# Kernel tuning notes

Hardware: AMD Instinct MI355X
Metric: run time of the kernel (lower is better)

Reference implementation:

```python
import jax, jax.numpy as jnp
import numpy as np

B, M, E = 8192, 200, 64
OTHER = 128
FEA = 256  # E + E + OTHER
ADIM = 3 * E


def setup_inputs() -> dict:
    key = jax.random.key(0)
    ks = jax.random.split(key, 12)
    s = lambda fan: 1.0 / np.sqrt(fan)
    return {
        "hist": jax.random.normal(ks[0], (B, M, E), jnp.float32),
        "target": jax.random.normal(ks[1], (B, E), jnp.float32),
        "other": jax.random.normal(ks[2], (B, OTHER), jnp.float32),
        "aW1": jax.random.normal(ks[3], (ADIM, ADIM // 2), jnp.float32) * s(ADIM),
        "ab1": jnp.zeros((ADIM // 2,), jnp.float32),
        "aW2": jax.random.normal(ks[4], (ADIM // 2, 1), jnp.float32) * s(ADIM // 2),
        "ab2": jnp.zeros((1,), jnp.float32),
        "oW1": jax.random.normal(ks[5], (FEA, FEA // 2), jnp.float32) * s(FEA),
        "ob1": jnp.zeros((FEA // 2,), jnp.float32),
        "oW2": jax.random.normal(ks[6], (FEA // 2, FEA // 3), jnp.float32) * s(FEA // 2),
        "ob2": jnp.zeros((FEA // 3,), jnp.float32),
        "oW3": jax.random.normal(ks[7], (FEA // 3, FEA // 4), jnp.float32) * s(FEA // 3),
        "ob3": jnp.zeros((FEA // 4,), jnp.float32),
        "fW": jax.random.normal(ks[8], (FEA // 4, 1), jnp.float32) * s(FEA // 4),
        "fb": jnp.zeros((1,), jnp.float32),
    }


def reference(hist, target, other, aW1, ab1, aW2, ab2,
              oW1, ob1, oW2, ob2, oW3, ob3, fW, fb):
    # DIN activation unit, vectorized over the m history steps.
    tgt = target[:, None, :]                                  # [B,1,E]
    a = jnp.concatenate(
        [hist, hist * tgt, jnp.broadcast_to(tgt, hist.shape)], axis=-1
    )                                                          # [B,M,3E]
    h = jax.nn.relu(jnp.einsum("bma,ah->bmh", a, aW1) + ab1)   # [B,M,3E/2]
    aij = jnp.einsum("bmh,ho->bmo", h, aW2) + ab2              # [B,M,1]
    tmp = jnp.sum(aij * hist, axis=1)                          # [B,E]

    x = jnp.concatenate([tmp, target, other], axis=1)          # [B,FEA]
    x = jax.nn.relu(x @ oW1 + ob1)
    x = jax.nn.relu(x @ oW2 + ob2)
    x = jax.nn.relu(x @ oW3 + ob3)
    out = jax.nn.sigmoid(x @ fW + fb)                          # [B,1]
    return out
```

## Files before the change

kernel.cpp:

```cpp
#include <hip/hip_runtime.h>
#include <math.h>

#define BATCH 8192
#define M 200
#define E 64
#define H1 96
#define F1 128
#define F2 85
#define F3 64
#define SH 72
#define MT 13

typedef _Float16 half8_t __attribute__((ext_vector_type(8)));
typedef float floatx4 __attribute__((ext_vector_type(4)));

__global__ __launch_bounds__(256, 4) void din_kernel(
    const float* __restrict__ hist, const float* __restrict__ target,
    const float* __restrict__ other,
    const float* __restrict__ aW1, const float* __restrict__ ab1,
    const float* __restrict__ aW2, const float* __restrict__ ab2,
    const float* __restrict__ oW1, const float* __restrict__ ob1,
    const float* __restrict__ oW2, const float* __restrict__ ob2,
    const float* __restrict__ oW3, const float* __restrict__ ob3,
    const float* __restrict__ fW,  const float* __restrict__ fb,
    float* __restrict__ out)
{
    __shared__ _Float16 WbT[H1 * SH];
    __shared__ float tgtS[E];
    __shared__ float beS[H1];
    __shared__ float aW2S[H1];
    __shared__ float xS[256];
    __shared__ float scr[512];
    __shared__ float h1S[F1];
    __shared__ float h2S[F2];
    __shared__ float ab2S;

    const int t = threadIdx.x;
    const int b = blockIdx.x;
    const int lane = t & 63;
    const int wv   = t >> 6;
    const int quad = lane >> 4;
    const int lm   = lane & 15;

    {
    }
    int mt = wv;
    const int row0  = mt * 16 + lm;
    const int rowc0 = row0 < M ? row0 : (M - 1);
    const float4* p0 = (const float4*)(hist + ((size_t)b * M + rowc0) * E + quad * 8);
    float4 f0 = p0[0], g0 = p0[1], f1 = p0[8], g1 = p0[9];
    float oth = 0.f;
    if (t >= 128) oth = other[(size_t)b * 128 + (t - 128)];

    if (t < E) tgtS[t] = target[(size_t)b * E + t];
    if (t == 0) ab2S = ab2[0];
    __syncthreads();

    for (int idx = t; idx < E * H1; idx += 256) {
        int k = idx / H1, j = idx - k * H1;
        float w = aW1[idx] + tgtS[k] * aW1[E * H1 + idx];
        WbT[j * SH + k] = (_Float16)w;
    }
    if (t < H1) {
        float s0 = ab1[t], s1 = 0.f, s2 = 0.f, s3 = 0.f;
        const float* wp = aW1 + (size_t)(2 * E) * H1 + t;
        #pragma unroll 4
        for (int k = 0; k < E; k += 4) {
            s0 += tgtS[k]     * wp[(size_t)k * H1];
            s1 += tgtS[k + 1] * wp[(size_t)(k + 1) * H1];
            s2 += tgtS[k + 2] * wp[(size_t)(k + 2) * H1];
            s3 += tgtS[k + 3] * wp[(size_t)(k + 3) * H1];
        }
        beS[t] = (s0 + s1) + (s2 + s3);
        aW2S[t] = aW2[t];
    }
    __syncthreads();

    half8_t bf[12];
    #pragma unroll
    for (int nt = 0; nt < 6; ++nt) {
        #pragma unroll
        for (int kk = 0; kk < 2; ++kk)
            bf[nt * 2 + kk] =
                *(const half8_t*)&WbT[(nt * 16 + lm) * SH + kk * 32 + quad * 8];
    }
    float beR[6], w2R[6];
    #pragma unroll
    for (int nt = 0; nt < 6; ++nt) {
        beR[nt] = beS[nt * 16 + lm];
        w2R[nt] = aW2S[nt * 16 + lm];
    }

    float tk0[8], tk1[8];
    #pragma unroll
    for (int j = 0; j < 8; ++j) { tk0[j] = 0.f; tk1[j] = 0.f; }

    const int qs16 = (lm >> 2) << 4;
    const int rsel = lm & 3;

    for (; mt < MT; mt += 4) {
        const int nmt = mt + 4;
        float4 nf0 = f0, ng0 = g0, nf1 = f1, ng1 = g1;
        if (nmt < MT) {
            const int nrow  = nmt * 16 + lm;
            const int nrowc = nrow < M ? nrow : (M - 1);
            const float4* np = (const float4*)(hist + ((size_t)b * M + nrowc) * E + quad * 8);
            nf0 = np[0]; ng0 = np[1]; nf1 = np[8]; ng1 = np[9];
        }

        const int m0  = mt * 16;
        const int row = m0 + lm;
        half8_t a0 = { (_Float16)f0.x, (_Float16)f0.y, (_Float16)f0.z, (_Float16)f0.w,
                       (_Float16)g0.x, (_Float16)g0.y, (_Float16)g0.z, (_Float16)g0.w };
        half8_t a1 = { (_Float16)f1.x, (_Float16)f1.y, (_Float16)f1.z, (_Float16)f1.w,
                       (_Float16)g1.x, (_Float16)g1.y, (_Float16)g1.z, (_Float16)g1.w };

        float s0 = 0.f, s1 = 0.f, s2 = 0.f, s3 = 0.f;
        #pragma unroll
        for (int nt = 0; nt < 6; ++nt) {
            floatx4 acc = {0.f, 0.f, 0.f, 0.f};
            acc = __builtin_amdgcn_mfma_f32_16x16x32_f16(a0, bf[nt * 2],     acc, 0, 0, 0);
            acc = __builtin_amdgcn_mfma_f32_16x16x32_f16(a1, bf[nt * 2 + 1], acc, 0, 0, 0);
            float be_n = beR[nt];
            float w2   = w2R[nt];
            s0 += fmaxf(acc[0] + be_n, 0.f) * w2;
            s1 += fmaxf(acc[1] + be_n, 0.f) * w2;
            s2 += fmaxf(acc[2] + be_n, 0.f) * w2;
            s3 += fmaxf(acc[3] + be_n, 0.f) * w2;
        }
        #pragma unroll
        for (int off = 1; off < 16; off <<= 1) {
            s0 += __shfl_xor(s0, off);
            s1 += __shfl_xor(s1, off);
            s2 += __shfl_xor(s2, off);
            s3 += __shfl_xor(s3, off);
        }
        float v0 = __shfl(s0, qs16), v1 = __shfl(s1, qs16);
        float v2 = __shfl(s2, qs16), v3 = __shfl(s3, qs16);
        float aij = (rsel == 0) ? v0 : (rsel == 1) ? v1 : (rsel == 2) ? v2 : v3;
        aij += ab2S;
        aij = (row < M) ? aij : 0.f;

        tk0[0] += f0.x * aij; tk0[1] += f0.y * aij;
        tk0[2] += f0.z * aij; tk0[3] += f0.w * aij;
        tk0[4] += g0.x * aij; tk0[5] += g0.y * aij;
        tk0[6] += g0.z * aij; tk0[7] += g0.w * aij;
        tk1[0] += f1.x * aij; tk1[1] += f1.y * aij;
        tk1[2] += f1.z * aij; tk1[3] += f1.w * aij;
        tk1[4] += g1.x * aij; tk1[5] += g1.y * aij;
        tk1[6] += g1.z * aij; tk1[7] += g1.w * aij;

        f0 = nf0; g0 = ng0; f1 = nf1; g1 = ng1;
    }

    #pragma unroll
    for (int j = 0; j < 8; ++j) {
        #pragma unroll
        for (int off = 1; off < 16; off <<= 1) {
            tk0[j] += __shfl_xor(tk0[j], off);
            tk1[j] += __shfl_xor(tk1[j], off);
        }
    }
    if (lm == 0) {
        #pragma unroll
        for (int j = 0; j < 8; ++j) {
            scr[wv * E + quad * 8 + j]      = tk0[j];
            scr[wv * E + 32 + quad * 8 + j] = tk1[j];
        }
    }
    __syncthreads();

    if (t < 64)
        xS[t] = (scr[t] + scr[64 + t]) + (scr[128 + t] + scr[192 + t]);
    else if (t < 128)
        xS[t] = tgtS[t - 64];
    else
        xS[t] = oth;
    __syncthreads();

    {
        const int g = t & 31, s = t >> 5;
        const float* wbase = oW1 + 4 * g;
        const int c0 = s * 32;
        float ax = 0.f, ay = 0.f, az = 0.f, aw = 0.f;
        #pragma unroll 8
        for (int i = 0; i < 32; ++i) {
            const int c = c0 + i;
            float xv = xS[c];
            float4 w4 = *(const float4*)(wbase + (size_t)c * F1);
            ax += xv * w4.x; ay += xv * w4.y;
            az += xv * w4.z; aw += xv * w4.w;
        }
        ax += __shfl_xor(ax, 32);
        ay += __shfl_xor(ay, 32);
        az += __shfl_xor(az, 32);
        aw += __shfl_xor(aw, 32);
        if (lane < 32) {
            float4 r = { ax, ay, az, aw };
            *(float4*)&scr[wv * 128 + 4 * g] = r;
        }
    }
    __syncthreads();
    if (t < F1)
        h1S[t] = fmaxf((scr[t] + scr[128 + t]) + (scr[256 + t] + scr[384 + t]) + ob1[t], 0.f);
    __syncthreads();

    {
        const int o = t & 127, ph = t >> 7;
        if (o < F2) {
            float sA = 0.f, sB = 0.f;
            const int c0 = ph * 64;
            #pragma unroll 8
            for (int c = 0; c < 64; c += 2) {
                sA += h1S[c0 + c]     * oW2[(size_t)(c0 + c) * F2 + o];
                sB += h1S[c0 + c + 1] * oW2[(size_t)(c0 + c + 1) * F2 + o];
            }
            scr[ph * 128 + o] = sA + sB;
        }
    }
    __syncthreads();
    if (t < F2) h2S[t] = fmaxf(scr[t] + scr[128 + t] + ob2[t], 0.f);
    __syncthreads();

    {
        const int o = t & 63, ph = t >> 6;
        const int c0 = (85 * ph) >> 2, c1 = (85 * (ph + 1)) >> 2;
        float s = 0.f;
        for (int c = c0; c < c1; ++c)
            s += h2S[c] * oW3[(size_t)c * F3 + o];
        scr[ph * 64 + o] = s;
    }
    __syncthreads();

    if (t < 64) {
        float v = fmaxf((scr[t] + scr[64 + t]) + (scr[128 + t] + scr[192 + t]) + ob3[t], 0.f) * fW[t];
        v += __shfl_xor(v, 1);  v += __shfl_xor(v, 2);  v += __shfl_xor(v, 4);
        v += __shfl_xor(v, 8);  v += __shfl_xor(v, 16); v += __shfl_xor(v, 32);
        if (t == 0) out[b] = 1.f / (1.f + __expf(-(v + fb[0])));
    }
}

extern "C" void kernel_launch(void* const* d_in, const int* in_sizes, int n_in,
                              void* d_out, int out_size, void* d_ws, size_t ws_size,
                              hipStream_t stream) {
    const float* hist   = (const float*)d_in[0];
    const float* target = (const float*)d_in[1];
    const float* other  = (const float*)d_in[2];
    const float* aW1    = (const float*)d_in[3];
    const float* ab1    = (const float*)d_in[4];
    const float* aW2    = (const float*)d_in[5];
    const float* ab2    = (const float*)d_in[6];
    const float* oW1    = (const float*)d_in[7];
    const float* ob1    = (const float*)d_in[8];
    const float* oW2    = (const float*)d_in[9];
    const float* ob2    = (const float*)d_in[10];
    const float* oW3    = (const float*)d_in[11];
    const float* ob3    = (const float*)d_in[12];
    const float* fW     = (const float*)d_in[13];
    const float* fb     = (const float*)d_in[14];
    float* out = (float*)d_out;

    din_kernel<<<BATCH, 256, 0, stream>>>(hist, target, other,
                                          aW1, ab1, aW2, ab2,
                                          oW1, ob1, oW2, ob2, oW3, ob3,
                                          fW, fb, out);
}
```

Baseline: 743.9 us.

## Process two history tiles per iteration and read MFMA B fragments from LDS

Each wave now loads and processes two 16-row history tiles per loop step, at rows mt and mt+64, and prefetches the next pair. This doubles the global loads in flight to hide memory latency. To pay for the extra registers, the MFMA B fragments, bias and aW2 values are read from shared memory inside the loop instead of being held in registers. The launch bounds are replaced with an explicit waves_per_eu(4,4) attribute. The cost is extra LDS reads per tile and some wasted clamped loads for rows past M.

```diff
diff --git a/kernel.cpp b/kernel.cpp
--- a/kernel.cpp
+++ b/kernel.cpp
@@ -14,7 +14,9 @@
 typedef _Float16 half8_t __attribute__((ext_vector_type(8)));
 typedef float floatx4 __attribute__((ext_vector_type(4)));
 
-__global__ __launch_bounds__(256, 4) void din_kernel(
+__global__ __launch_bounds__(256)
+__attribute__((amdgpu_waves_per_eu(4, 4)))
+void din_kernel(
     const float* __restrict__ hist, const float* __restrict__ target,
     const float* __restrict__ other,
     const float* __restrict__ aW1, const float* __restrict__ ab1,
@@ -42,13 +44,13 @@
     const int quad = lane >> 4;
     const int lm   = lane & 15;
 
-    {
-    }
-    int mt = wv;
-    const int row0  = mt * 16 + lm;
-    const int rowc0 = row0 < M ? row0 : (M - 1);
-    const float4* p0 = (const float4*)(hist + ((size_t)b * M + rowc0) * E + quad * 8);
-    float4 f0 = p0[0], g0 = p0[1], f1 = p0[8], g1 = p0[9];
+    const float* histB = hist + (size_t)b * M * E + quad * 8;
+    int rowA = wv * 16 + lm;
+    int rowB = rowA + 64;
+    const float4* pA = (const float4*)(histB + (size_t)(rowA < M ? rowA : M - 1) * E);
+    const float4* pB = (const float4*)(histB + (size_t)(rowB < M ? rowB : M - 1) * E);
+    float4 fA0 = pA[0], gA0 = pA[1], fA1 = pA[8], gA1 = pA[9];
+    float4 fB0 = pB[0], gB0 = pB[1], fB1 = pB[8], gB1 = pB[9];
     float oth = 0.f;
     if (t >= 128) oth = other[(size_t)b * 128 + (t - 128)];
 
@@ -76,53 +78,30 @@
     }
     __syncthreads();
 
-    half8_t bf[12];
-    #pragma unroll
-    for (int nt = 0; nt < 6; ++nt) {
-        #pragma unroll
-        for (int kk = 0; kk < 2; ++kk)
-            bf[nt * 2 + kk] =
-                *(const half8_t*)&WbT[(nt * 16 + lm) * SH + kk * 32 + quad * 8];
-    }
-    float beR[6], w2R[6];
-    #pragma unroll
-    for (int nt = 0; nt < 6; ++nt) {
-        beR[nt] = beS[nt * 16 + lm];
-        w2R[nt] = aW2S[nt * 16 + lm];
-    }
+    const _Float16* bfB = &WbT[lm * SH + quad * 8];
+    const int qs16 = (lm >> 2) << 4;
+    const int rsel = lm & 3;
 
     float tk0[8], tk1[8];
     #pragma unroll
     for (int j = 0; j < 8; ++j) { tk0[j] = 0.f; tk1[j] = 0.f; }
 
-    const int qs16 = (lm >> 2) << 4;
-    const int rsel = lm & 3;
-
-    for (; mt < MT; mt += 4) {
-        const int nmt = mt + 4;
-        float4 nf0 = f0, ng0 = g0, nf1 = f1, ng1 = g1;
-        if (nmt < MT) {
-            const int nrow  = nmt * 16 + lm;
-            const int nrowc = nrow < M ? nrow : (M - 1);
-            const float4* np = (const float4*)(hist + ((size_t)b * M + nrowc) * E + quad * 8);
-            nf0 = np[0]; ng0 = np[1]; nf1 = np[8]; ng1 = np[9];
-        }
-
-        const int m0  = mt * 16;
-        const int row = m0 + lm;
+    auto tile_aij = [&](const float4& f0, const float4& g0,
+                        const float4& f1, const float4& g1, int row) -> float {
         half8_t a0 = { (_Float16)f0.x, (_Float16)f0.y, (_Float16)f0.z, (_Float16)f0.w,
                        (_Float16)g0.x, (_Float16)g0.y, (_Float16)g0.z, (_Float16)g0.w };
         half8_t a1 = { (_Float16)f1.x, (_Float16)f1.y, (_Float16)f1.z, (_Float16)f1.w,
                        (_Float16)g1.x, (_Float16)g1.y, (_Float16)g1.z, (_Float16)g1.w };
-
         float s0 = 0.f, s1 = 0.f, s2 = 0.f, s3 = 0.f;
         #pragma unroll
         for (int nt = 0; nt < 6; ++nt) {
+            half8_t b0 = *(const half8_t*)(bfB + nt * (16 * SH));
+            half8_t b1 = *(const half8_t*)(bfB + nt * (16 * SH) + 32);
             floatx4 acc = {0.f, 0.f, 0.f, 0.f};
-            acc = __builtin_amdgcn_mfma_f32_16x16x32_f16(a0, bf[nt * 2],     acc, 0, 0, 0);
-            acc = __builtin_amdgcn_mfma_f32_16x16x32_f16(a1, bf[nt * 2 + 1], acc, 0, 0, 0);
-            float be_n = beR[nt];
-            float w2   = w2R[nt];
+            acc = __builtin_amdgcn_mfma_f32_16x16x32_f16(a0, b0, acc, 0, 0, 0);
+            acc = __builtin_amdgcn_mfma_f32_16x16x32_f16(a1, b1, acc, 0, 0, 0);
+            float be_n = beS[nt * 16 + lm];
+            float w2   = aW2S[nt * 16 + lm];
             s0 += fmaxf(acc[0] + be_n, 0.f) * w2;
             s1 += fmaxf(acc[1] + be_n, 0.f) * w2;
             s2 += fmaxf(acc[2] + be_n, 0.f) * w2;
@@ -139,18 +118,46 @@
         float v2 = __shfl(s2, qs16), v3 = __shfl(s3, qs16);
         float aij = (rsel == 0) ? v0 : (rsel == 1) ? v1 : (rsel == 2) ? v2 : v3;
         aij += ab2S;
-        aij = (row < M) ? aij : 0.f;
-
-        tk0[0] += f0.x * aij; tk0[1] += f0.y * aij;
-        tk0[2] += f0.z * aij; tk0[3] += f0.w * aij;
-        tk0[4] += g0.x * aij; tk0[5] += g0.y * aij;
-        tk0[6] += g0.z * aij; tk0[7] += g0.w * aij;
-        tk1[0] += f1.x * aij; tk1[1] += f1.y * aij;
-        tk1[2] += f1.z * aij; tk1[3] += f1.w * aij;
-        tk1[4] += g1.x * aij; tk1[5] += g1.y * aij;
-        tk1[6] += g1.z * aij; tk1[7] += g1.w * aij;
-
-        f0 = nf0; g0 = ng0; f1 = nf1; g1 = ng1;
+        return (row < M) ? aij : 0.f;
+    };
+
+    for (int mt = wv; mt < MT; mt += 8) {
+        const int nmt = mt + 8;
+        float4 nfA0 = fA0, ngA0 = gA0, nfA1 = fA1, ngA1 = gA1;
+        float4 nfB0 = fB0, ngB0 = gB0, nfB1 = fB1, ngB1 = gB1;
+        if (nmt < MT) {
+            int nrA = nmt * 16 + lm;
+            int nrB = nrA + 64;
+            const float4* npA = (const float4*)(histB + (size_t)(nrA < M ? nrA : M - 1) * E);
+            const float4* npB = (const float4*)(histB + (size_t)(nrB < M ? nrB : M - 1) * E);
+            nfA0 = npA[0]; ngA0 = npA[1]; nfA1 = npA[8]; ngA1 = npA[9];
+            nfB0 = npB[0]; ngB0 = npB[1]; nfB1 = npB[8]; ngB1 = npB[9];
+        }
+
+        const float aijA = tile_aij(fA0, gA0, fA1, gA1, rowA);
+        tk0[0] += fA0.x * aijA; tk0[1] += fA0.y * aijA;
+        tk0[2] += fA0.z * aijA; tk0[3] += fA0.w * aijA;
+        tk0[4] += gA0.x * aijA; tk0[5] += gA0.y * aijA;
+        tk0[6] += gA0.z * aijA; tk0[7] += gA0.w * aijA;
+        tk1[0] += fA1.x * aijA; tk1[1] += fA1.y * aijA;
+        tk1[2] += fA1.z * aijA; tk1[3] += fA1.w * aijA;
+        tk1[4] += gA1.x * aijA; tk1[5] += gA1.y * aijA;
+        tk1[6] += gA1.z * aijA; tk1[7] += gA1.w * aijA;
+
+        const float aijB = tile_aij(fB0, gB0, fB1, gB1, rowB);
+        tk0[0] += fB0.x * aijB; tk0[1] += fB0.y * aijB;
+        tk0[2] += fB0.z * aijB; tk0[3] += fB0.w * aijB;
+        tk0[4] += gB0.x * aijB; tk0[5] += gB0.y * aijB;
+        tk0[6] += gB0.z * aijB; tk0[7] += gB0.w * aijB;
+        tk1[0] += fB1.x * aijB; tk1[1] += fB1.y * aijB;
+        tk1[2] += fB1.z * aijB; tk1[3] += fB1.w * aijB;
+        tk1[4] += gB1.x * aijB; tk1[5] += gB1.y * aijB;
+        tk1[6] += gB1.z * aijB; tk1[7] += gB1.w * aijB;
+
+        fA0 = nfA0; gA0 = ngA0; fA1 = nfA1; gA1 = ngA1;
+        fB0 = nfB0; gB0 = ngB0; fB1 = nfB1; gB1 = ngB1;
+        rowA = nmt * 16 + lm;
+        rowB = rowA + 64;
     }
 
     #pragma unroll
```

After: 1.178 ms. 58.4% more time.

## Precompute transposed fp16 attention weights once and double MFMAs instead of per-block fold

Applied to the files above, without the earlier changes.

Adds a small prep kernel that converts the hist and hist*target slices of aW1 to transposed fp16 once into workspace, so each batch block no longer builds a target-folded weight tile in shared memory. The main kernel now forms hist*target in registers and issues four MFMAs per output tile instead of two, reading weights from global/L2 each iteration rather than holding them in registers. The software prefetch of the next hist tile is removed and the occupancy hint in launch bounds is dropped. The trade is less per-block setup and LDS work against twice the matrix ops and repeated weight loads inside the loop.

```diff
diff --git a/kernel.cpp b/kernel.cpp
--- a/kernel.cpp
+++ b/kernel.cpp
@@ -8,15 +8,24 @@
 #define F1 128
 #define F2 85
 #define F3 64
-#define SH 72
 #define MT 13
 
 typedef _Float16 half8_t __attribute__((ext_vector_type(8)));
 typedef float floatx4 __attribute__((ext_vector_type(4)));
 
-__global__ __launch_bounds__(256, 4) void din_kernel(
+__global__ void din_prep(const float* __restrict__ aW1,
+                         _Float16* __restrict__ waT, _Float16* __restrict__ wbT)
+{
+    const int n = blockIdx.x;
+    const int k = threadIdx.x;
+    waT[n * 64 + k] = (_Float16)aW1[(size_t)k * H1 + n];
+    wbT[n * 64 + k] = (_Float16)aW1[(size_t)(E + k) * H1 + n];
+}
+
+__global__ __launch_bounds__(256) void din_kernel(
     const float* __restrict__ hist, const float* __restrict__ target,
     const float* __restrict__ other,
+    const _Float16* __restrict__ waT, const _Float16* __restrict__ wbT,
     const float* __restrict__ aW1, const float* __restrict__ ab1,
     const float* __restrict__ aW2, const float* __restrict__ ab2,
     const float* __restrict__ oW1, const float* __restrict__ ob1,
@@ -25,7 +34,6 @@
     const float* __restrict__ fW,  const float* __restrict__ fb,
     float* __restrict__ out)
 {
-    __shared__ _Float16 WbT[H1 * SH];
     __shared__ float tgtS[E];
     __shared__ float beS[H1];
     __shared__ float aW2S[H1];
@@ -42,25 +50,12 @@
     const int quad = lane >> 4;
     const int lm   = lane & 15;
 
-    {
-    }
-    int mt = wv;
-    const int row0  = mt * 16 + lm;
-    const int rowc0 = row0 < M ? row0 : (M - 1);
-    const float4* p0 = (const float4*)(hist + ((size_t)b * M + rowc0) * E + quad * 8);
-    float4 f0 = p0[0], g0 = p0[1], f1 = p0[8], g1 = p0[9];
     float oth = 0.f;
     if (t >= 128) oth = other[(size_t)b * 128 + (t - 128)];
-
     if (t < E) tgtS[t] = target[(size_t)b * E + t];
     if (t == 0) ab2S = ab2[0];
     __syncthreads();
 
-    for (int idx = t; idx < E * H1; idx += 256) {
-        int k = idx / H1, j = idx - k * H1;
-        float w = aW1[idx] + tgtS[k] * aW1[E * H1 + idx];
-        WbT[j * SH + k] = (_Float16)w;
-    }
     if (t < H1) {
         float s0 = ab1[t], s1 = 0.f, s2 = 0.f, s3 = 0.f;
         const float* wp = aW1 + (size_t)(2 * E) * H1 + t;
@@ -76,53 +71,52 @@
     }
     __syncthreads();
 
-    half8_t bf[12];
-    #pragma unroll
-    for (int nt = 0; nt < 6; ++nt) {
-        #pragma unroll
-        for (int kk = 0; kk < 2; ++kk)
-            bf[nt * 2 + kk] =
-                *(const half8_t*)&WbT[(nt * 16 + lm) * SH + kk * 32 + quad * 8];
-    }
-    float beR[6], w2R[6];
-    #pragma unroll
-    for (int nt = 0; nt < 6; ++nt) {
-        beR[nt] = beS[nt * 16 + lm];
-        w2R[nt] = aW2S[nt * 16 + lm];
-    }
+    const float* histB = hist + (size_t)b * M * E + quad * 8;
+    const _Float16* waB = waT + lm * 64 + quad * 8;
+    const _Float16* wbB = wbT + lm * 64 + quad * 8;
+    const float4* tgt4 = (const float4*)tgtS;
+    const int qs16 = (lm >> 2) << 4;
+    const int rsel = lm & 3;
 
     float tk0[8], tk1[8];
     #pragma unroll
     for (int j = 0; j < 8; ++j) { tk0[j] = 0.f; tk1[j] = 0.f; }
 
-    const int qs16 = (lm >> 2) << 4;
-    const int rsel = lm & 3;
-
-    for (; mt < MT; mt += 4) {
-        const int nmt = mt + 4;
-        float4 nf0 = f0, ng0 = g0, nf1 = f1, ng1 = g1;
-        if (nmt < MT) {
-            const int nrow  = nmt * 16 + lm;
-            const int nrowc = nrow < M ? nrow : (M - 1);
-            const float4* np = (const float4*)(hist + ((size_t)b * M + nrowc) * E + quad * 8);
-            nf0 = np[0]; ng0 = np[1]; nf1 = np[8]; ng1 = np[9];
-        }
-
-        const int m0  = mt * 16;
-        const int row = m0 + lm;
+    for (int mt = wv; mt < MT; mt += 4) {
+        const int row = mt * 16 + lm;
+        const float4* p = (const float4*)(histB + (size_t)(row < M ? row : M - 1) * E);
+        float4 f0 = p[0], g0 = p[1], f1 = p[8], g1 = p[9];
+
+        float4 T0 = tgt4[quad * 2],     T1 = tgt4[quad * 2 + 1];
+        float4 T2 = tgt4[8 + quad * 2], T3 = tgt4[9 + quad * 2];
+
         half8_t a0 = { (_Float16)f0.x, (_Float16)f0.y, (_Float16)f0.z, (_Float16)f0.w,
                        (_Float16)g0.x, (_Float16)g0.y, (_Float16)g0.z, (_Float16)g0.w };
         half8_t a1 = { (_Float16)f1.x, (_Float16)f1.y, (_Float16)f1.z, (_Float16)f1.w,
                        (_Float16)g1.x, (_Float16)g1.y, (_Float16)g1.z, (_Float16)g1.w };
+        half8_t a0t = { (_Float16)(f0.x * T0.x), (_Float16)(f0.y * T0.y),
+                        (_Float16)(f0.z * T0.z), (_Float16)(f0.w * T0.w),
+                        (_Float16)(g0.x * T1.x), (_Float16)(g0.y * T1.y),
+                        (_Float16)(g0.z * T1.z), (_Float16)(g0.w * T1.w) };
+        half8_t a1t = { (_Float16)(f1.x * T2.x), (_Float16)(f1.y * T2.y),
+                        (_Float16)(f1.z * T2.z), (_Float16)(f1.w * T2.w),
+                        (_Float16)(g1.x * T3.x), (_Float16)(g1.y * T3.y),
+                        (_Float16)(g1.z * T3.z), (_Float16)(g1.w * T3.w) };
 
         float s0 = 0.f, s1 = 0.f, s2 = 0.f, s3 = 0.f;
         #pragma unroll
         for (int nt = 0; nt < 6; ++nt) {
+            half8_t wa0 = *(const half8_t*)(waB + nt * 1024);
+            half8_t wa1 = *(const half8_t*)(waB + nt * 1024 + 32);
+            half8_t wb0 = *(const half8_t*)(wbB + nt * 1024);
+            half8_t wb1 = *(const half8_t*)(wbB + nt * 1024 + 32);
             floatx4 acc = {0.f, 0.f, 0.f, 0.f};
-            acc = __builtin_amdgcn_mfma_f32_16x16x32_f16(a0, bf[nt * 2],     acc, 0, 0, 0);
-            acc = __builtin_amdgcn_mfma_f32_16x16x32_f16(a1, bf[nt * 2 + 1], acc, 0, 0, 0);
-            float be_n = beR[nt];
-            float w2   = w2R[nt];
+            acc = __builtin_amdgcn_mfma_f32_16x16x32_f16(a0,  wa0, acc, 0, 0, 0);
+            acc = __builtin_amdgcn_mfma_f32_16x16x32_f16(a1,  wa1, acc, 0, 0, 0);
+            acc = __builtin_amdgcn_mfma_f32_16x16x32_f16(a0t, wb0, acc, 0, 0, 0);
+            acc = __builtin_amdgcn_mfma_f32_16x16x32_f16(a1t, wb1, acc, 0, 0, 0);
+            float be_n = beS[nt * 16 + lm];
+            float w2   = aW2S[nt * 16 + lm];
             s0 += fmaxf(acc[0] + be_n, 0.f) * w2;
             s1 += fmaxf(acc[1] + be_n, 0.f) * w2;
             s2 += fmaxf(acc[2] + be_n, 0.f) * w2;
@@ -149,8 +143,6 @@
         tk1[2] += f1.z * aij; tk1[3] += f1.w * aij;
         tk1[4] += g1.x * aij; tk1[5] += g1.y * aij;
         tk1[6] += g1.z * aij; tk1[7] += g1.w * aij;
-
-        f0 = nf0; g0 = ng0; f1 = nf1; g1 = ng1;
     }
 
     #pragma unroll
@@ -260,7 +252,12 @@
     const float* fb     = (const float*)d_in[14];
     float* out = (float*)d_out;
 
+    _Float16* waT = (_Float16*)d_ws;
+    _Float16* wbT = waT + H1 * E;
+
+    din_prep<<<H1, E, 0, stream>>>(aW1, waT, wbT);
     din_kernel<<<BATCH, 256, 0, stream>>>(hist, target, other,
+                                          waT, wbT,
                                           aW1, ab1, aW2, ab2,
                                           oW1, ob1, oW2, ob2, oW3, ob3,
                                           fW, fb, out);
```

Result: slower. 785.3 us (+5.6%).
